# Optimization experiments

Hardware: AMD Instinct MI355X
Metric: run time of the kernel (lower is better)

Reference implementation:

```python
import jax, jax.numpy as jnp
import numpy as np
from jax import lax

S = 30      # num_sensors
FD = 200    # feature_dim
T = 1024    # signal length
B = 1024    # batch
NC = 7      # num_classes


def setup_inputs() -> dict:
    key = jax.random.key(0)
    ks = jax.random.split(key, 24)
    rn = lambda i, shape: jax.random.normal(ks[i], shape, jnp.float32) * 0.05
    # normalized adjacency with self-loops: D^-1/2 (A+I) D^-1/2
    rng = np.random.default_rng(0)
    A = (rng.random((S, S)) > 0.7).astype(np.float32)
    A = ((A + A.T) > 0).astype(np.float32)
    A_self = A + np.eye(S, dtype=np.float32)
    dinv = 1.0 / np.sqrt(A_self.sum(1))
    adj_self = jnp.asarray(dinv[:, None] * A_self * dinv[None, :])
    return dict(
        x=jax.random.normal(ks[0], (B, S, T), jnp.float32),
        adj_self=adj_self,
        Wc1=rn(1, (S, S, 3)), bc1=jnp.zeros((S,), jnp.float32),
        Wc2=rn(2, (S, S, 3)), bc2=jnp.zeros((S,), jnp.float32),
        Wt=rn(3, (T, FD)), bt=jnp.zeros((FD,), jnp.float32),
        Wa=rn(4, (FD, FD)),
        Wm1=rn(5, (FD, FD)), Wm2=rn(6, (FD, FD)), Wm3=rn(7, (FD, FD)),
        Wg1=rn(8, (FD, FD)), Wg2=rn(9, (FD, FD)),
        wg=rn(10, (FD, 3)),
        Wp1=rn(11, (FD, FD // 2)), Wp2=rn(12, (FD, FD // 2)), Wp3=rn(13, (FD, FD // 2)),
        Wl=rn(14, (FD, 150)), Wgl=rn(15, (FD, 150)),
        Ws1=rn(16, (S, S // 2)), Ws2=rn(17, (S // 2, S)),
        Wf1=rn(18, (300, 150)), Wf2=rn(19, (150, 300)),
        Wcls=rn(20, (S * 600, NC)), bcls=jnp.zeros((NC,), jnp.float32),
    )


def reference(x, adj_self, Wc1, bc1, Wc2, bc2, Wt, bt, Wa, Wm1, Wm2, Wm3,
              Wg1, Wg2, wg, Wp1, Wp2, Wp3, Wl, Wgl, Ws1, Ws2, Wf1, Wf2,
              Wcls, bcls):
    dn = ('NCH', 'OIH', 'NCH')
    # CNN feature extractor: [B,S,T] -> [B,S,FD]
    h = jax.nn.relu(lax.conv_general_dilated(x, Wc1, (1,), 'SAME', dimension_numbers=dn) + bc1[None, :, None])
    h = jax.nn.relu(lax.conv_general_dilated(h, Wc2, (1,), 'SAME', dimension_numbers=dn) + bc2[None, :, None])
    F2 = jax.nn.relu(jnp.einsum('bst,tf->bsf', h, Wt) + bt)
    # MGCN: learned feature adjacency + 3-order GCN (batched, replaces per-sample loop)
    A_F = jax.nn.softmax(jax.nn.relu(jnp.einsum('bif,fg,bjg->bij', F2, Wa, F2)), axis=-1)
    gc = lambda A, X, W: jax.nn.relu(jnp.einsum('bij,bjf,fg->big', A, X, W))
    x1 = gc(A_F, F2, Wm1)
    x2 = gc(A_F, x1, Wm2)
    x3 = gc(A_F, x2, Wm3)
    # signal GCN on physical adjacency (2-layer, eval mode so dropout is identity)
    h1 = jax.nn.relu(jnp.einsum('ij,bjf,fg->big', adj_self, F2, Wg1))
    x_sensor = jnp.einsum('ij,bjf,fg->big', adj_self, h1, Wg2)
    H1 = (x1 + x_sensor) * 0.5
    H2 = (x2 + x_sensor) * 0.5
    H3 = (x3 + x_sensor) * 0.5
    # adaptive aggregation: per-node softmax gate over 3 branches, project to FD//2 each -> 300
    scores = jnp.stack([jnp.einsum('bsf,f->bs', H, wg[:, k]) for k, H in enumerate((H1, H2, H3))], -1)
    g = jax.nn.softmax(scores, -1)  # [B,S,3]
    agg = lambda k, H, Wp: jnp.einsum('ij,bjf,fg->big', adj_self, g[..., k:k + 1] * H, Wp)
    G_h = jnp.concatenate([agg(0, H1, Wp1), agg(1, H2, Wp2), agg(2, H3, Wp3)], -1)  # [B,S,300]
    # LGFM: local (physical adj) + global (learned adj) -> 150+150
    loc = jax.nn.relu(jnp.einsum('ij,bjf,fg->big', adj_self, F2, Wl))
    glb = jax.nn.relu(jnp.einsum('bij,bjf,fg->big', A_F, F2, Wgl))
    G_v = jnp.concatenate([loc, glb], -1)  # [B,S,300]
    # cross squeeze-excitation: channel SE on G_h driven by G_v, feature SE on G_v driven by G_h
    wch = jax.nn.sigmoid(jax.nn.relu(G_v.mean(-1) @ Ws1) @ Ws2)   # [B,S]
    G_h_att = G_h * wch[:, :, None]
    wft = jax.nn.sigmoid(jax.nn.relu(G_h.mean(1) @ Wf1) @ Wf2)    # [B,300]
    G_v_att = G_v * wft[:, None, :]
    G = jnp.concatenate([G_h_att, G_v_att], -1).reshape(x.shape[0], -1)  # [B, S*600]
    return jax.nn.log_softmax(G @ Wcls + bcls, axis=-1)
```

## Files before the change

### kernel.cpp

```cpp
#include <hip/hip_runtime.h>
#include <math.h>

#define S   30
#define FD  200
#define TT  1024
#define BB  1024
#define NC  7

#define OFS_C1   0ull
#define OFS_F2   31457280ull
#define OFS_AF   0ull
#define OFS_GV   921600ull
#define OFS_GH   10137600ull
#define OFS_R    19691520ull
#define OFS_WT   28907520ull

__global__ __launch_bounds__(256) void k_conv1(
    const float* __restrict__ x,
    const float* __restrict__ Wc1, const float* __restrict__ bc1,
    float* __restrict__ C1) {
    const int c = blockIdx.x, b = blockIdx.y;
    const int t = threadIdx.x;
    const int t0 = c * 256;
    __shared__ float xb[S * 258];
// ... 77 lines not shown
__device__ inline void gemm_w4_pf(const float* Xl, int xstr, const float* __restrict__ W,
                                  int ct, int rt, float acc[][4]) {
    const float* wp = W + 4 * ct;
    float4 wreg[8];
#pragma unroll
    for (int u = 0; u < 8; u++) wreg[u] = *(const float4*)(wp + u * N);
#pragma unroll 1
    for (int kt = 0; kt < K / 8 - 1; kt++) {
        float4 wnxt[8];
#pragma unroll
        for (int u = 0; u < 8; u++) wnxt[u] = *(const float4*)(wp + (kt * 8 + 8 + u) * N);
#pragma unroll
        for (int m = 0; m < RPT; m++) {
            const float* xr = Xl + (rt * RPT + m) * xstr + kt * 8;
            float4 a0 = *(const float4*)(xr);
            float4 a1 = *(const float4*)(xr + 4);
            fma_tile8(a0, a1, wreg, acc[m]);
        }
#pragma unroll
        for (int u = 0; u < 8; u++) wreg[u] = wnxt[u];
    }
    {
        const int kb = K - 8;
#pragma unroll
        for (int m = 0; m < RPT; m++) {
            const float* xr = Xl + (rt * RPT + m) * xstr + kb;
            float4 a0 = *(const float4*)(xr);
            float4 a1 = *(const float4*)(xr + 4);
            fma_tile8(a0, a1, wreg, acc[m]);
        }
    }
}

template<int RPT, int N, int K>
__device__ inline void gemm_w4_pf_dual(const float* X0, const float* X1, int xstr,
                                       const float* __restrict__ W,
                                       int ct, int rt,
                                       float acc0[][4], float acc1[][4]) {
    const float* wp = W + 4 * ct;
    float4 wreg[8];
#pragma unroll
    for (int u = 0; u < 8; u++) wreg[u] = *(const float4*)(wp + u * N);
#pragma unroll 1
    for (int kt = 0; kt < K / 8 - 1; kt++) {
        float4 wnxt[8];
#pragma unroll
        for (int u = 0; u < 8; u++) wnxt[u] = *(const float4*)(wp + (kt * 8 + 8 + u) * N);
#pragma unroll
        for (int m = 0; m < RPT; m++) {
            const float* xr = X0 + (rt * RPT + m) * xstr + kt * 8;
            float4 a0 = *(const float4*)(xr);
            float4 a1 = *(const float4*)(xr + 4);
            fma_tile8(a0, a1, wreg, acc0[m]);
        }
#pragma unroll
        for (int m = 0; m < RPT; m++) {
            const float* xr = X1 + (rt * RPT + m) * xstr + kt * 8;
            float4 a0 = *(const float4*)(xr);
            float4 a1 = *(const float4*)(xr + 4);
            fma_tile8(a0, a1, wreg, acc1[m]);
        }
#pragma unroll
        for (int u = 0; u < 8; u++) wreg[u] = wnxt[u];
    }
    {
        const int kb = K - 8;
#pragma unroll
        for (int m = 0; m < RPT; m++) {
            const float* xr = X0 + (rt * RPT + m) * xstr + kb;
            float4 a0 = *(const float4*)(xr);
            float4 a1 = *(const float4*)(xr + 4);
            fma_tile8(a0, a1, wreg, acc0[m]);
        }
#pragma unroll
        for (int m = 0; m < RPT; m++) {
            const float* xr = X1 + (rt * RPT + m) * xstr + kb;
            float4 a0 = *(const float4*)(xr);
            float4 a1 = *(const float4*)(xr + 4);
            fma_tile8(a0, a1, wreg, acc1[m]);
        }
    }
}

template<int RPT>
__device__ inline void gemm_a32(const float* Al, const float* Xl, int xstr,
                                int ct, int rt, float acc[][4]) {
#pragma unroll
    for (int k4 = 0; k4 < 8; k4++) {
        float4 xv0 = *(const float4*)(Xl + (4 * k4 + 0) * xstr + 4 * ct);
        float4 xv1 = *(const float4*)(Xl + (4 * k4 + 1) * xstr + 4 * ct);
        float4 xv2 = *(const float4*)(Xl + (4 * k4 + 2) * xstr + 4 * ct);
        float4 xv3 = *(const float4*)(Xl + (4 * k4 + 3) * xstr + 4 * ct);
#pragma unroll
        for (int m = 0; m < RPT; m++) {
            float4 av = *(const float4*)(Al + (rt * RPT + m) * 32 + 4 * k4);
            FMA4(av.x, xv0, acc[m]);
            FMA4(av.y, xv1, acc[m]);
            FMA4(av.z, xv2, acc[m]);
            FMA4(av.w, xv3, acc[m]);
        }
    }
}

template<int RPT>
__device__ inline void gemm_a32_dual(const float* Al0, const float* X0,
                                     const float* Al1, const float* X1,
                                     int xstr, int ct, int rt,
                                     float acc0[][4], float acc1[][4]) {
#pragma unroll
    for (int k4 = 0; k4 < 8; k4++) {
        float4 x00 = *(const float4*)(X0 + (4 * k4 + 0) * xstr + 4 * ct);
        float4 x01 = *(const float4*)(X0 + (4 * k4 + 1) * xstr + 4 * ct);
        float4 x02 = *(const float4*)(X0 + (4 * k4 + 2) * xstr + 4 * ct);
        float4 x03 = *(const float4*)(X0 + (4 * k4 + 3) * xstr + 4 * ct);
        float4 x10 = *(const float4*)(X1 + (4 * k4 + 0) * xstr + 4 * ct);
        float4 x11 = *(const float4*)(X1 + (4 * k4 + 1) * xstr + 4 * ct);
        float4 x12 = *(const float4*)(X1 + (4 * k4 + 2) * xstr + 4 * ct);
        float4 x13 = *(const float4*)(X1 + (4 * k4 + 3) * xstr + 4 * ct);
#pragma unroll
        for (int m = 0; m < RPT; m++) {
            float4 av0 = *(const float4*)(Al0 + (rt * RPT + m) * 32 + 4 * k4);
            FMA4(av0.x, x00, acc0[m]);
            FMA4(av0.y, x01, acc0[m]);
            FMA4(av0.z, x02, acc0[m]);
            FMA4(av0.w, x03, acc0[m]);
            float4 av1 = *(const float4*)(Al1 + (rt * RPT + m) * 32 + 4 * k4);
            FMA4(av1.x, x10, acc1[m]);
            FMA4(av1.y, x11, acc1[m]);
            FMA4(av1.z, x12, acc1[m]);
            FMA4(av1.w, x13, acc1[m]);
        }
    }
}

__device__ inline void gemm_w150_pf(const float* Xl, const float* __restrict__ W,
                                    int ct2, int rt2, float acc[5][4], int off23) {
    const float* wp = W + 4 * ct2;
    float2 wa[8], wb[8];
#pragma unroll
    for (int u = 0; u < 8; u++) {
        wa[u] = *(const float2*)(wp + u * 150);
        wb[u] = *(const float2*)(wp + u * 150 + off23);
    }
#pragma unroll 1
    for (int kt = 0; kt < 24; kt++) {
        float2 na[8], nb[8];
#pragma unroll
        for (int u = 0; u < 8; u++) {
            int k = kt * 8 + 8 + u;
            na[u] = *(const float2*)(wp + k * 150);
            nb[u] = *(const float2*)(wp + k * 150 + off23);
        }
#pragma unroll
        for (int m = 0; m < 5; m++) {
            const float* xr = Xl + (rt2 * 5 + m) * FD + kt * 8;
            float4 a0 = *(const float4*)(xr);
            float4 a1 = *(const float4*)(xr + 4);
            float av[8] = {a0.x, a0.y, a0.z, a0.w, a1.x, a1.y, a1.z, a1.w};
#pragma unroll
            for (int u = 0; u < 8; u++) {
                acc[m][0] = fmaf(av[u], wa[u].x, acc[m][0]);
                acc[m][1] = fmaf(av[u], wa[u].y, acc[m][1]);
                acc[m][2] = fmaf(av[u], wb[u].x, acc[m][2]);
                acc[m][3] = fmaf(av[u], wb[u].y, acc[m][3]);
            }
        }
#pragma unroll
        for (int u = 0; u < 8; u++) { wa[u] = na[u]; wb[u] = nb[u]; }
    }
#pragma unroll
    for (int m = 0; m < 5; m++) {
        const float* xr = Xl + (rt2 * 5 + m) * FD + 192;
        float4 a0 = *(const float4*)(xr);
        float4 a1 = *(const float4*)(xr + 4);
        float av[8] = {a0.x, a0.y, a0.z, a0.w, a1.x, a1.y, a1.z, a1.w};
#pragma unroll
        for (int u = 0; u < 8; u++) {
            acc[m][0] = fmaf(av[u], wa[u].x, acc[m][0]);
            acc[m][1] = fmaf(av[u], wa[u].y, acc[m][1]);
            acc[m][2] = fmaf(av[u], wb[u].x, acc[m][2]);
            acc[m][3] = fmaf(av[u], wb[u].y, acc[m][3]);
        }
    }
}

__device__ inline void gemm_w150_pf_dual(const float* X0, const float* X1,
                                         const float* __restrict__ W,
                                         int ct2, int rt2,
                                         float acc0[5][4], float acc1[5][4], int off23) {
    const float* wp = W + 4 * ct2;
    float2 wa[8], wb[8];
#pragma unroll
    for (int u = 0; u < 8; u++) {
        wa[u] = *(const float2*)(wp + u * 150);
        wb[u] = *(const float2*)(wp + u * 150 + off23);
    }
#pragma unroll 1
    for (int kt = 0; kt < 24; kt++) {
        float2 na[8], nb[8];
#pragma unroll
        for (int u = 0; u < 8; u++) {
            int k = kt * 8 + 8 + u;
            na[u] = *(const float2*)(wp + k * 150);
            nb[u] = *(const float2*)(wp + k * 150 + off23);
        }
#pragma unroll
        for (int m = 0; m < 5; m++) {
            const float* xr = X0 + (rt2 * 5 + m) * FD + kt * 8;
            float4 a0 = *(const float4*)(xr);
            float4 a1 = *(const float4*)(xr + 4);
            float av[8] = {a0.x, a0.y, a0.z, a0.w, a1.x, a1.y, a1.z, a1.w};
#pragma unroll
            for (int u = 0; u < 8; u++) {
// ... 229 lines not shown
        float den = 0.f;
        for (int j = 0; j < S; j++) den += expf(scl0[t * 32 + j] - mx);
        float inv = 1.f / den;
        for (int j = 0; j < S; j++) scl0[t * 32 + j] = expf(scl0[t * 32 + j] - mx) * inv;
    } else if (t >= 64 && t < 64 + S) {
        int s = t - 64;
        float mx = -1e30f;
        for (int j = 0; j < S; j++) mx = fmaxf(mx, scl1[s * 32 + j]);
        float den = 0.f;
        for (int j = 0; j < S; j++) den += expf(scl1[s * 32 + j] - mx);
        float inv = 1.f / den;
        for (int j = 0; j < S; j++) scl1[s * 32 + j] = expf(scl1[s * 32 + j] - mx) * inv;
    }
    __syncthreads();
    for (int idx = t; idx < S * S; idx += 256) {
        int i = idx / S, j = idx % S;
        AF[(size_t)b0 * S * S + idx] = scl0[i * 32 + j];
        AF[(size_t)b1 * S * S + idx] = scl1[i * 32 + j];
    }
    zacc<6>(acc0); zacc<6>(acc1);
    if (t < 250) gemm_a32_dual<6>(adjl, A0, adjl, A1, FD, ct, rt, acc0, acc1);
    __syncthreads();
    if (t < 250) {
#pragma unroll
        for (int m = 0; m < 6; m++) {
            float4 o0 = {acc0[m][0], acc0[m][1], acc0[m][2], acc0[m][3]};
            float4 o1 = {acc1[m][0], acc1[m][1], acc1[m][2], acc1[m][3]};
            *(float4*)(Bu0 + (rt * 6 + m) * FD + 4 * ct) = o0;
            *(float4*)(Bu1 + (rt * 6 + m) * FD + 4 * ct) = o1;
        }
    }
    __syncthreads();
    const int ct2 = t % 38, rt2 = t / 38;
    const bool full = (4 * ct2 + 2) < 150;
    const int off23 = full ? 2 : -2;
    if (t < 228) {
        float a20[5][4], a21[5][4];
        zacc<5>(a20); zacc<5>(a21);
        gemm_w150_pf_dual(Bu0, Bu1, Wl, ct2, rt2, a20, a21, off23);
#pragma unroll
        for (int m = 0; m < 5; m++) {
            float* o0 = Gv + (size_t)(b0 * S + rt2 * 5 + m) * 300 + 4 * ct2;
            float* o1 = Gv + (size_t)(b1 * S + rt2 * 5 + m) * 300 + 4 * ct2;
            o0[0] = fmaxf(a20[m][0], 0.f); o0[1] = fmaxf(a20[m][1], 0.f);
            o1[0] = fmaxf(a21[m][0], 0.f); o1[1] = fmaxf(a21[m][1], 0.f);
            if (full) {
                o0[2] = fmaxf(a20[m][2], 0.f); o0[3] = fmaxf(a20[m][3], 0.f);
                o1[2] = fmaxf(a21[m][2], 0.f); o1[3] = fmaxf(a21[m][3], 0.f);
            }
        }
    }
    __syncthreads();
    zacc<6>(acc0); zacc<6>(acc1);
    if (t < 250) gemm_a32_dual<6>(scl0, A0, scl1, A1, FD, ct, rt, acc0, acc1);
    __syncthreads();
    if (t < 250) {
#pragma unroll
        for (int m = 0; m < 6; m++) {
            float4 o0 = {acc0[m][0], acc0[m][1], acc0[m][2], acc0[m][3]};
            float4 o1 = {acc1[m][0], acc1[m][1], acc1[m][2], acc1[m][3]};
            *(float4*)(Bu0 + (rt * 6 + m) * FD + 4 * ct) = o0;
            *(float4*)(Bu1 + (rt * 6 + m) * FD + 4 * ct) = o1;
        }
    }
    __syncthreads();
    if (t < 228) {
        float a20[5][4], a21[5][4];
        zacc<5>(a20); zacc<5>(a21);
        gemm_w150_pf_dual(Bu0, Bu1, Wgl, ct2, rt2, a20, a21, off23);
#pragma unroll
        for (int m = 0; m < 5; m++) {
            float* o0 = Gv + (size_t)(b0 * S + rt2 * 5 + m) * 300 + 150 + 4 * ct2;
            float* o1 = Gv + (size_t)(b1 * S + rt2 * 5 + m) * 300 + 150 + 4 * ct2;
            o0[0] = fmaxf(a20[m][0], 0.f); o0[1] = fmaxf(a20[m][1], 0.f);
            o1[0] = fmaxf(a21[m][0], 0.f); o1[1] = fmaxf(a21[m][1], 0.f);
            if (full) {
                o0[2] = fmaxf(a20[m][2], 0.f); o0[3] = fmaxf(a20[m][3], 0.f);
                o1[2] = fmaxf(a21[m][2], 0.f); o1[3] = fmaxf(a21[m][3], 0.f);
            }
        }
    }
}

__global__ __launch_bounds__(256, 2) void k_mgcn(
    const float* __restrict__ F2g, const float* __restrict__ AFg,
    const float* __restrict__ adj,
    const float* __restrict__ Wg1, const float* __restrict__ Wg2,
    const float* __restrict__ Wm1, const float* __restrict__ Wm2,
    const float* __restrict__ Wm3, const float* __restrict__ wg,
    const float* __restrict__ Wp1, const float* __restrict__ Wp2,
    const float* __restrict__ Wp3,
    float* __restrict__ Rws, float* __restrict__ Gh) {
    const int b0 = blockIdx.x * 2, b1 = b0 + 1;
    const int t = threadIdx.x;
    __shared__ float A0[32 * FD], A1[32 * FD];
    __shared__ float afl0[1024], afl1[1024];
    __shared__ float adjl[1024];
    __shared__ float sk[192];
    __shared__ float gl[192];
    const int ct = t % 50, rt = t / 50;
    const int ct3 = t % 25, rt3 = t / 25;

    for (int idx = t; idx < 1500; idx += 256) {
        *(float4*)(A0 + 4 * idx) = *(const float4*)(F2g + (size_t)b0 * S * FD + 4 * idx);
        *(float4*)(A1 + 4 * idx) = *(const float4*)(F2g + (size_t)b1 * S * FD + 4 * idx);
    }
    for (int idx = t; idx < 400; idx += 256) { A0[6000 + idx] = 0.f; A1[6000 + idx] = 0.f; }
    for (int idx = t; idx < 1024; idx += 256) {
        int r = idx >> 5, cc = idx & 31;
        bool in = (r < S && cc < S);
        afl0[idx] = in ? AFg[(size_t)b0 * S * S + r * S + cc] : 0.f;
        afl1[idx] = in ? AFg[(size_t)b1 * S * S + r * S + cc] : 0.f;
        adjl[idx] = in ? adj[r * S + cc] : 0.f;
    }
    if (t < 192) sk[t] = 0.f;
    __syncthreads();

    float acc0[6][4], acc1[6][4], xsr0[6][4], xsr1[6][4];

#define DZ() { zacc<6>(acc0); zacc<6>(acc1); }
#define DWRITE(RELU)                                                        \
    if (t < 250) {                                                          \
        _Pragma("unroll")                                                   \
        for (int m = 0; m < 6; m++) {                                       \
            float4 o0, o1;                                                  \
            o0.x = RELU ? fmaxf(acc0[m][0], 0.f) : acc0[m][0];              \
            o0.y = RELU ? fmaxf(acc0[m][1], 0.f) : acc0[m][1];              \
            o0.z = RELU ? fmaxf(acc0[m][2], 0.f) : acc0[m][2];              \
            o0.w = RELU ? fmaxf(acc0[m][3], 0.f) : acc0[m][3];              \
            o1.x = RELU ? fmaxf(acc1[m][0], 0.f) : acc1[m][0];              \
            o1.y = RELU ? fmaxf(acc1[m][1], 0.f) : acc1[m][1];              \
            o1.z = RELU ? fmaxf(acc1[m][2], 0.f) : acc1[m][2];              \
            o1.w = RELU ? fmaxf(acc1[m][3], 0.f) : acc1[m][3];              \
            *(float4*)(A0 + (rt * 6 + m) * FD + 4 * ct) = o0;               \
            *(float4*)(A1 + (rt * 6 + m) * FD + 4 * ct) = o1;               \
        }                                                                   \
    }

    DZ();
    if (t < 250) gemm_a32_dual<6>(adjl, A0, adjl, A1, FD, ct, rt, acc0, acc1);
    __syncthreads();
    DWRITE(false);
    __syncthreads();
    DZ();
    if (t < 250) gemm_w4_pf_dual<6, FD, FD>(A0, A1, FD, Wg1, ct, rt, acc0, acc1);
    __syncthreads();
    DWRITE(true);
    __syncthreads();
    DZ();
    if (t < 250) gemm_a32_dual<6>(adjl, A0, adjl, A1, FD, ct, rt, acc0, acc1);
    __syncthreads();
    DWRITE(false);
    __syncthreads();
    DZ();
    if (t < 250) gemm_w4_pf_dual<6, FD, FD>(A0, A1, FD, Wg2, ct, rt, acc0, acc1);
    __syncthreads();
#pragma unroll
    for (int m = 0; m < 6; m++) {
#pragma unroll
        for (int q = 0; q < 4; q++) { xsr0[m][q] = acc0[m][q]; xsr1[m][q] = acc1[m][q]; }
    }
    for (int idx = t; idx < 1500; idx += 256) {
        *(float4*)(A0 + 4 * idx) = *(const float4*)(F2g + (size_t)b0 * S * FD + 4 * idx);
        *(float4*)(A1 + 4 * idx) = *(const float4*)(F2g + (size_t)b1 * S * FD + 4 * idx);
    }
    __syncthreads();

    const float* Wm[3] = {Wm1, Wm2, Wm3};
    const float* Wp[3] = {Wp1, Wp2, Wp3};
#pragma unroll 1
    for (int k = 0; k < 3; k++) {
        DZ();
        if (t < 250) gemm_a32_dual<6>(afl0, A0, afl1, A1, FD, ct, rt, acc0, acc1);
        __syncthreads();
        DWRITE(false);
        __syncthreads();
        DZ();
        if (t < 250) gemm_w4_pf_dual<6, FD, FD>(A0, A1, FD, Wm[k], ct, rt, acc0, acc1);
        __syncthreads();
        if (t < 250) {
#pragma unroll
            for (int m = 0; m < 6; m++) {
#pragma unroll
                for (int q = 0; q < 4; q++) {
                    acc0[m][q] = fmaxf(acc0[m][q], 0.f);
                    acc1[m][q] = fmaxf(acc1[m][q], 0.f);
                }
            }
#pragma unroll
            for (int m = 0; m < 6; m++) {
                int row = rt * 6 + m;
                float wg0 = wg[(4 * ct + 0) * 3 + k], wg1v = wg[(4 * ct + 1) * 3 + k];
                float wg2v = wg[(4 * ct + 2) * 3 + k], wg3 = wg[(4 * ct + 3) * 3 + k];
                float h00 = 0.5f * (acc0[m][0] + xsr0[m][0]);
                float h01 = 0.5f * (acc0[m][1] + xsr0[m][1]);
                float h02 = 0.5f * (acc0[m][2] + xsr0[m][2]);
                float h03 = 0.5f * (acc0[m][3] + xsr0[m][3]);
                float4 o0 = {h00, h01, h02, h03};
                *(float4*)(A0 + row * FD + 4 * ct) = o0;
                atomicAdd(&sk[row * 3 + k],
                          h00 * wg0 + h01 * wg1v + h02 * wg2v + h03 * wg3);
                float h10 = 0.5f * (acc1[m][0] + xsr1[m][0]);
                float h11 = 0.5f * (acc1[m][1] + xsr1[m][1]);
                float h12 = 0.5f * (acc1[m][2] + xsr1[m][2]);
                float h13 = 0.5f * (acc1[m][3] + xsr1[m][3]);
                float4 o1 = {h10, h11, h12, h13};
                *(float4*)(A1 + row * FD + 4 * ct) = o1;
                atomicAdd(&sk[96 + row * 3 + k],
                          h10 * wg0 + h11 * wg1v + h12 * wg2v + h13 * wg3);
            }
        }
        __syncthreads();
        if (t < 250) {
            float a30[3][4], a31[3][4];
            zacc<3>(a30); zacc<3>(a31);
            gemm_w4_pf_dual<3, 100, FD>(A0, A1, FD, Wp[k], ct3, rt3, a30, a31);
#pragma unroll
            for (int m = 0; m < 3; m++) {
                float4 o0 = {a30[m][0], a30[m][1], a30[m][2], a30[m][3]};
                float4 o1 = {a31[m][0], a31[m][1], a31[m][2], a31[m][3]};
                *(float4*)(Rws + ((size_t)(k * BB + b0) * S + rt3 * 3 + m) * 100 + 4 * ct3) = o0;
                *(float4*)(Rws + ((size_t)(k * BB + b1) * S + rt3 * 3 + m) * 100 + 4 * ct3) = o1;
            }
        }
        __syncthreads();
        if (k < 2) {
            DWRITE(false);
            __syncthreads();
        }
    }

    if (t < S) {
        float a0 = sk[t * 3 + 0], a1 = sk[t * 3 + 1], a2 = sk[t * 3 + 2];
        float m = fmaxf(a0, fmaxf(a1, a2));
        float e0 = expf(a0 - m), e1 = expf(a1 - m), e2 = expf(a2 - m);
        float inv = 1.f / (e0 + e1 + e2);
        gl[t * 3 + 0] = e0 * inv; gl[t * 3 + 1] = e1 * inv; gl[t * 3 + 2] = e2 * inv;
    } else if (t >= 64 && t < 64 + S) {
        int s = t - 64;
        float a0 = sk[96 + s * 3 + 0], a1 = sk[96 + s * 3 + 1], a2 = sk[96 + s * 3 + 2];
        float m = fmaxf(a0, fmaxf(a1, a2));
        float e0 = expf(a0 - m), e1 = expf(a1 - m), e2 = expf(a2 - m);
        float inv = 1.f / (e0 + e1 + e2);
        gl[96 + s * 3 + 0] = e0 * inv; gl[96 + s * 3 + 1] = e1 * inv; gl[96 + s * 3 + 2] = e2 * inv;
    }
    __syncthreads();

#pragma unroll 1
    for (int k = 0; k < 3; k++) {
        for (int idx = t; idx < S * 100; idx += 256) {
            int row = idx / 100, col = idx % 100;
            A0[row * FD + col] = Rws[((size_t)(k * BB + b0) * S) * 100 + idx];
            A1[row * FD + col] = Rws[((size_t)(k * BB + b1) * S) * 100 + idx];
        }
        for (int idx = t; idx < 1024; idx += 256) {
            int cc = idx & 31;
            afl0[idx] = (cc < S) ? adjl[idx] * gl[cc * 3 + k] : 0.f;
            afl1[idx] = (cc < S) ? adjl[idx] * gl[96 + cc * 3 + k] : 0.f;
        }
        __syncthreads();
        if (t < 250) {
            float a30[3][4], a31[3][4];
            zacc<3>(a30); zacc<3>(a31);
            gemm_a32_dual<3>(afl0, A0, afl1, A1, FD, ct3, rt3, a30, a31);
#pragma unroll
            for (int m = 0; m < 3; m++) {
                float4 o0 = {a30[m][0], a30[m][1], a30[m][2], a30[m][3]};
                float4 o1 = {a31[m][0], a31[m][1], a31[m][2], a31[m][3]};
                *(float4*)(Gh + (size_t)(b0 * S + rt3 * 3 + m) * 300 + k * 100 + 4 * ct3) = o0;
                *(float4*)(Gh + (size_t)(b1 * S + rt3 * 3 + m) * 300 + k * 100 + 4 * ct3) = o1;
            }
        }
        __syncthreads();
    }
#undef DZ
#undef DWRITE
}

__global__ __launch_bounds__(256) void k_tw(const float* __restrict__ Wcls,
                                            float* __restrict__ WclsT) {
    int idx = blockIdx.x * 256 + threadIdx.x;
    if (idx < S * 600 * NC) {
        int i = idx / NC, c = idx % NC;
        WclsT[c * (S * 600) + i] = Wcls[idx];
    }
}

__global__ __launch_bounds__(256) void k_secls(
    const float* __restrict__ Gh, const float* __restrict__ Gv,
    const float* __restrict__ Ws1, const float* __restrict__ Ws2,
    const float* __restrict__ Wf1, const float* __restrict__ Wf2,
    const float* __restrict__ WclsT, const float* __restrict__ bcls,
    float* __restrict__ out) {
    const int b = blockIdx.x, t = threadIdx.x;
    __shared__ float red[NC][256];
    __shared__ float mrow[S];
    __shared__ float u[15];
    __shared__ float mb[300];
    __shared__ float v[150];
    __shared__ float wftl[300];
    __shared__ float wchl[S];
    if (t < S) {
        float a = 0.f;
        const float* gp = Gv + ((size_t)b * S + t) * 300;
        for (int j = 0; j < 300; j++) a += gp[j];
        mrow[t] = a * (1.f / 300.f);
    }
    for (int j = t; j < 300; j += 256) {
        float a = 0.f;
        for (int s = 0; s < S; s++) a += Gh[(size_t)b * S * 300 + s * 300 + j];
        mb[j] = a * (1.f / S);
    }
    __syncthreads();
    if (t < 15) {
        float a = 0.f;
        for (int i = 0; i < S; i++) a += mrow[i] * Ws1[i * 15 + t];
        u[t] = fmaxf(a, 0.f);
    }
    if (t >= 64 && t < 64 + 150) {
        int h = t - 64;
        float a = 0.f;
        for (int j = 0; j < 300; j++) a += mb[j] * Wf1[j * 150 + h];
        v[h] = fmaxf(a, 0.f);
    }
    __syncthreads();
    if (t < S) {
        float a = 0.f;
        for (int h = 0; h < 15; h++) a += u[h] * Ws2[h * 30 + t];
        wchl[t] = 1.f / (1.f + expf(-a));
    }
    for (int j = t; j < 300; j += 256) {
        float a = 0.f;
        for (int h = 0; h < 150; h++) a += v[h] * Wf2[h * 300 + j];
        wftl[j] = 1.f / (1.f + expf(-a));
    }
    __syncthreads();
    float acc[NC];
#pragma unroll
    for (int c = 0; c < NC; c++) acc[c] = 0.f;
    for (int i = t; i < S * 600; i += 256) {
        int s = i / 600, j = i % 600;
        float gval = (j < 300)
            ? Gh[(size_t)b * S * 300 + s * 300 + j] * wchl[s]
            : Gv[(size_t)b * S * 300 + s * 300 + (j - 300)] * wftl[j - 300];
#pragma unroll
        for (int c = 0; c < NC; c++)
            acc[c] = fmaf(gval, WclsT[c * (S * 600) + i], acc[c]);
    }
#pragma unroll
    for (int c = 0; c < NC; c++) red[c][t] = acc[c];
    __syncthreads();
    for (int off = 128; off > 0; off >>= 1) {
        if (t < off) {
#pragma unroll
            for (int c = 0; c < NC; c++) red[c][t] += red[c][t + off];
        }
        __syncthreads();
    }
    if (t == 0) {
        float lg[NC];
        float mx = -1e30f;
#pragma unroll
        for (int c = 0; c < NC; c++) { lg[c] = red[c][0] + bcls[c]; mx = fmaxf(mx, lg[c]); }
        float den = 0.f;
#pragma unroll
        for (int c = 0; c < NC; c++) den += expf(lg[c] - mx);
        float lden = logf(den) + mx;
#pragma unroll
        for (int c = 0; c < NC; c++) out[b * NC + c] = lg[c] - lden;
    }
}

extern "C" void kernel_launch(void* const* d_in, const int* in_sizes, int n_in,
                              void* d_out, int out_size, void* d_ws, size_t ws_size,
                              hipStream_t stream) {
    const float* x    = (const float*)d_in[0];
    const float* adj  = (const float*)d_in[1];
    const float* Wc1  = (const float*)d_in[2];
    const float* bc1  = (const float*)d_in[3];
    const float* Wc2  = (const float*)d_in[4];
    const float* bc2  = (const float*)d_in[5];
    const float* Wt   = (const float*)d_in[6];
    const float* bt   = (const float*)d_in[7];
    const float* Wa   = (const float*)d_in[8];
    const float* Wm1  = (const float*)d_in[9];
    const float* Wm2  = (const float*)d_in[10];
    const float* Wm3  = (const float*)d_in[11];
    const float* Wg1  = (const float*)d_in[12];
    const float* Wg2  = (const float*)d_in[13];
    const float* wg   = (const float*)d_in[14];
    const float* Wp1  = (const float*)d_in[15];
    const float* Wp2  = (const float*)d_in[16];
    const float* Wp3  = (const float*)d_in[17];
    const float* Wl   = (const float*)d_in[18];
    const float* Wgl  = (const float*)d_in[19];
    const float* Ws1  = (const float*)d_in[20];
    const float* Ws2  = (const float*)d_in[21];
    const float* Wf1  = (const float*)d_in[22];
    const float* Wf2  = (const float*)d_in[23];
    const float* Wcls = (const float*)d_in[24];
    const float* bcls = (const float*)d_in[25];

    float* ws    = (float*)d_ws;
    float* C1    = ws + OFS_C1;
    float* F2    = ws + OFS_F2;
    float* AF    = ws + OFS_AF;
    float* GV    = ws + OFS_GV;
    float* GH    = ws + OFS_GH;
    float* RWS   = ws + OFS_R;
    float* WCLST = ws + OFS_WT;
    float* out   = (float*)d_out;

    k_conv1<<<dim3(4, BB), 256, 0, stream>>>(x, Wc1, bc1, C1);
    k_f2d<<<BB / 2, 256, 0, stream>>>(C1, Wc2, bc2, Wt, bt, F2);
    k_tw<<<(S * 600 * NC + 255) / 256, 256, 0, stream>>>(Wcls, WCLST);
    k_att2<<<BB / 2, 256, 0, stream>>>(F2, Wa, adj, Wl, Wgl, AF, GV);
    k_mgcn<<<BB / 2, 256, 0, stream>>>(F2, AF, adj, Wg1, Wg2, Wm1, Wm2, Wm3, wg,
                                       Wp1, Wp2, Wp3, RWS, GH);
    k_secls<<<BB, 256, 0, stream>>>(GH, GV, Ws1, Ws2, Wf1, Wf2, WCLST, bcls, out);
}
```

Before: 1.135 ms.

## Process four batch samples per block in MGCN kernel to reuse weight loads

The MGCN kernel now handles four samples per block instead of two, with quad variants of the adjacency and weight GEMM helpers so each prefetched weight tile feeds four samples. This halves weight traffic per sample and halves the block count. In exchange, shared memory rises to about 120 KB and register pressure roughly doubles (four accumulator sets plus four saved residuals), so launch bounds drop to one block per SM. Only 256 blocks are launched, which risks spills and poor occupancy.

```diff
diff --git a/kernel.cpp b/kernel.cpp
--- a/kernel.cpp
+++ b/kernel.cpp
@@ -183,6 +183,70 @@
     }
 }
 
+template<int RPT, int N, int K>
+__device__ inline void gemm_w4_pf_quad(const float* X0, const float* X1,
+                                       const float* X2, const float* X3, int xstr,
+                                       const float* __restrict__ W,
+                                       int ct, int rt,
+                                       float acc0[][4], float acc1[][4],
+                                       float acc2[][4], float acc3[][4]) {
+    const float* wp = W + 4 * ct;
+    float4 wreg[8];
+#pragma unroll
+    for (int u = 0; u < 8; u++) wreg[u] = *(const float4*)(wp + u * N);
+#pragma unroll 1
+    for (int kt = 0; kt < K / 8 - 1; kt++) {
+        float4 wnxt[8];
+#pragma unroll
+        for (int u = 0; u < 8; u++) wnxt[u] = *(const float4*)(wp + (kt * 8 + 8 + u) * N);
+#pragma unroll
+        for (int m = 0; m < RPT; m++) {
+            const float* xr = X0 + (rt * RPT + m) * xstr + kt * 8;
+            fma_tile8(*(const float4*)(xr), *(const float4*)(xr + 4), wreg, acc0[m]);
+        }
+#pragma unroll
+        for (int m = 0; m < RPT; m++) {
+            const float* xr = X1 + (rt * RPT + m) * xstr + kt * 8;
+            fma_tile8(*(const float4*)(xr), *(const float4*)(xr + 4), wreg, acc1[m]);
+        }
+#pragma unroll
+        for (int m = 0; m < RPT; m++) {
+            const float* xr = X2 + (rt * RPT + m) * xstr + kt * 8;
+            fma_tile8(*(const float4*)(xr), *(const float4*)(xr + 4), wreg, acc2[m]);
+        }
+#pragma unroll
+        for (int m = 0; m < RPT; m++) {
+            const float* xr = X3 + (rt * RPT + m) * xstr + kt * 8;
+            fma_tile8(*(const float4*)(xr), *(const float4*)(xr + 4), wreg, acc3[m]);
+        }
+#pragma unroll
+        for (int u = 0; u < 8; u++) wreg[u] = wnxt[u];
+    }
+    {
+        const int kb = K - 8;
+#pragma unroll
+        for (int m = 0; m < RPT; m++) {
+            const float* xr = X0 + (rt * RPT + m) * xstr + kb;
+            fma_tile8(*(const float4*)(xr), *(const float4*)(xr + 4), wreg, acc0[m]);
+        }
+#pragma unroll
+        for (int m = 0; m < RPT; m++) {
+            const float* xr = X1 + (rt * RPT + m) * xstr + kb;
+            fma_tile8(*(const float4*)(xr), *(const float4*)(xr + 4), wreg, acc1[m]);
+        }
+#pragma unroll
+        for (int m = 0; m < RPT; m++) {
+            const float* xr = X2 + (rt * RPT + m) * xstr + kb;
+            fma_tile8(*(const float4*)(xr), *(const float4*)(xr + 4), wreg, acc2[m]);
+        }
+#pragma unroll
+        for (int m = 0; m < RPT; m++) {
+            const float* xr = X3 + (rt * RPT + m) * xstr + kb;
+            fma_tile8(*(const float4*)(xr), *(const float4*)(xr + 4), wreg, acc3[m]);
+        }
+    }
+}
+
 template<int RPT>
 __device__ inline void gemm_a32(const float* Al, const float* Xl, int xstr,
                                 int ct, int rt, float acc[][4]) {
@@ -230,6 +294,75 @@
             FMA4(av1.y, x11, acc1[m]);
             FMA4(av1.z, x12, acc1[m]);
             FMA4(av1.w, x13, acc1[m]);
+        }
+    }
+}
+
+template<int RPT>
+__device__ inline void gemm_a32_quad(const float* Al0, const float* X0,
+                                     const float* Al1, const float* X1,
+                                     const float* Al2, const float* X2,
+                                     const float* Al3, const float* X3,
+                                     int xstr, int ct, int rt,
+                                     float acc0[][4], float acc1[][4],
+                                     float acc2[][4], float acc3[][4]) {
+#pragma unroll
+    for (int k4 = 0; k4 < 8; k4++) {
+        {
+            float4 x0 = *(const float4*)(X0 + (4 * k4 + 0) * xstr + 4 * ct);
+            float4 x1 = *(const float4*)(X0 + (4 * k4 + 1) * xstr + 4 * ct);
+            float4 x2 = *(const float4*)(X0 + (4 * k4 + 2) * xstr + 4 * ct);
+            float4 x3 = *(const float4*)(X0 + (4 * k4 + 3) * xstr + 4 * ct);
+#pragma unroll
+            for (int m = 0; m < RPT; m++) {
+                float4 av = *(const float4*)(Al0 + (rt * RPT + m) * 32 + 4 * k4);
+                FMA4(av.x, x0, acc0[m]);
+                FMA4(av.y, x1, acc0[m]);
+                FMA4(av.z, x2, acc0[m]);
+                FMA4(av.w, x3, acc0[m]);
+            }
+        }
+        {
+            float4 x0 = *(const float4*)(X1 + (4 * k4 + 0) * xstr + 4 * ct);
+            float4 x1 = *(const float4*)(X1 + (4 * k4 + 1) * xstr + 4 * ct);
+            float4 x2 = *(const float4*)(X1 + (4 * k4 + 2) * xstr + 4 * ct);
+            float4 x3 = *(const float4*)(X1 + (4 * k4 + 3) * xstr + 4 * ct);
+#pragma unroll
+            for (int m = 0; m < RPT; m++) {
+                float4 av = *(const float4*)(Al1 + (rt * RPT + m) * 32 + 4 * k4);
+                FMA4(av.x, x0, acc1[m]);
+                FMA4(av.y, x1, acc1[m]);
+                FMA4(av.z, x2, acc1[m]);
+                FMA4(av.w, x3, acc1[m]);
+            }
+        }
+        {
+            float4 x0 = *(const float4*)(X2 + (4 * k4 + 0) * xstr + 4 * ct);
+            float4 x1 = *(const float4*)(X2 + (4 * k4 + 1) * xstr + 4 * ct);
+            float4 x2 = *(const float4*)(X2 + (4 * k4 + 2) * xstr + 4 * ct);
+            float4 x3 = *(const float4*)(X2 + (4 * k4 + 3) * xstr + 4 * ct);
+#pragma unroll
+            for (int m = 0; m < RPT; m++) {
+                float4 av = *(const float4*)(Al2 + (rt * RPT + m) * 32 + 4 * k4);
+                FMA4(av.x, x0, acc2[m]);
+                FMA4(av.y, x1, acc2[m]);
+                FMA4(av.z, x2, acc2[m]);
+                FMA4(av.w, x3, acc2[m]);
+            }
+        }
+        {
+            float4 x0 = *(const float4*)(X3 + (4 * k4 + 0) * xstr + 4 * ct);
+            float4 x1 = *(const float4*)(X3 + (4 * k4 + 1) * xstr + 4 * ct);
+            float4 x2 = *(const float4*)(X3 + (4 * k4 + 2) * xstr + 4 * ct);
+            float4 x3 = *(const float4*)(X3 + (4 * k4 + 3) * xstr + 4 * ct);
+#pragma unroll
+            for (int m = 0; m < RPT; m++) {
+                float4 av = *(const float4*)(Al3 + (rt * RPT + m) * 32 + 4 * k4);
+                FMA4(av.x, x0, acc3[m]);
+                FMA4(av.y, x1, acc3[m]);
+                FMA4(av.z, x2, acc3[m]);
+                FMA4(av.w, x3, acc3[m]);
+            }
         }
     }
 }
@@ -625,7 +758,7 @@
     }
 }
 
-__global__ __launch_bounds__(256, 2) void k_mgcn(
+__global__ __launch_bounds__(256, 1) void k_mgcn4(
     const float* __restrict__ F2g, const float* __restrict__ AFg,
     const float* __restrict__ adj,
     const float* __restrict__ Wg1, const float* __restrict__ Wg2,
@@ -634,39 +767,47 @@
     const float* __restrict__ Wp1, const float* __restrict__ Wp2,
     const float* __restrict__ Wp3,
     float* __restrict__ Rws, float* __restrict__ Gh) {
-    const int b0 = blockIdx.x * 2, b1 = b0 + 1;
+    const int b0 = blockIdx.x * 4;
     const int t = threadIdx.x;
-    __shared__ float A0[32 * FD], A1[32 * FD];
-    __shared__ float afl0[1024], afl1[1024];
+    __shared__ float A0[32 * FD], A1[32 * FD], A2[32 * FD], A3[32 * FD];
+    __shared__ float afl0[1024], afl1[1024], afl2[1024], afl3[1024];
     __shared__ float adjl[1024];
-    __shared__ float sk[192];
-    __shared__ float gl[192];
+    __shared__ float sk[384];
+    __shared__ float gl[384];
     const int ct = t % 50, rt = t / 50;
     const int ct3 = t % 25, rt3 = t / 25;
 
     for (int idx = t; idx < 1500; idx += 256) {
-        *(float4*)(A0 + 4 * idx) = *(const float4*)(F2g + (size_t)b0 * S * FD + 4 * idx);
-        *(float4*)(A1 + 4 * idx) = *(const float4*)(F2g + (size_t)b1 * S * FD + 4 * idx);
-    }
-    for (int idx = t; idx < 400; idx += 256) { A0[6000 + idx] = 0.f; A1[6000 + idx] = 0.f; }
+        *(float4*)(A0 + 4 * idx) = *(const float4*)(F2g + (size_t)(b0 + 0) * S * FD + 4 * idx);
+        *(float4*)(A1 + 4 * idx) = *(const float4*)(F2g + (size_t)(b0 + 1) * S * FD + 4 * idx);
+        *(float4*)(A2 + 4 * idx) = *(const float4*)(F2g + (size_t)(b0 + 2) * S * FD + 4 * idx);
+        *(float4*)(A3 + 4 * idx) = *(const float4*)(F2g + (size_t)(b0 + 3) * S * FD + 4 * idx);
+    }
+    for (int idx = t; idx < 400; idx += 256) {
+        A0[6000 + idx] = 0.f; A1[6000 + idx] = 0.f;
+        A2[6000 + idx] = 0.f; A3[6000 + idx] = 0.f;
+    }
     for (int idx = t; idx < 1024; idx += 256) {
         int r = idx >> 5, cc = idx & 31;
         bool in = (r < S && cc < S);
-        afl0[idx] = in ? AFg[(size_t)b0 * S * S + r * S + cc] : 0.f;
-        afl1[idx] = in ? AFg[(size_t)b1 * S * S + r * S + cc] : 0.f;
+        afl0[idx] = in ? AFg[(size_t)(b0 + 0) * S * S + r * S + cc] : 0.f;
+        afl1[idx] = in ? AFg[(size_t)(b0 + 1) * S * S + r * S + cc] : 0.f;
+        afl2[idx] = in ? AFg[(size_t)(b0 + 2) * S * S + r * S + cc] : 0.f;
+        afl3[idx] = in ? AFg[(size_t)(b0 + 3) * S * S + r * S + cc] : 0.f;
         adjl[idx] = in ? adj[r * S + cc] : 0.f;
     }
-    if (t < 192) sk[t] = 0.f;
-    __syncthreads();
-
-    float acc0[6][4], acc1[6][4], xsr0[6][4], xsr1[6][4];
-
-#define DZ() { zacc<6>(acc0); zacc<6>(acc1); }
-#define DWRITE(RELU)                                                        \
+    for (int idx = t; idx < 384; idx += 256) sk[idx] = 0.f;
+    __syncthreads();
+
+    float acc0[6][4], acc1[6][4], acc2[6][4], acc3[6][4];
+    float xsr0[6][4], xsr1[6][4], xsr2[6][4], xsr3[6][4];
+
+#define QZ() { zacc<6>(acc0); zacc<6>(acc1); zacc<6>(acc2); zacc<6>(acc3); }
+#define QWRITE(RELU)                                                        \
     if (t < 250) {                                                          \
         _Pragma("unroll")                                                   \
         for (int m = 0; m < 6; m++) {                                       \
-            float4 o0, o1;                                                  \
+            float4 o0, o1, o2, o3;                                          \
             o0.x = RELU ? fmaxf(acc0[m][0], 0.f) : acc0[m][0];              \
             o0.y = RELU ? fmaxf(acc0[m][1], 0.f) : acc0[m][1];              \
             o0.z = RELU ? fmaxf(acc0[m][2], 0.f) : acc0[m][2];              \
@@ -675,37 +816,56 @@
             o1.y = RELU ? fmaxf(acc1[m][1], 0.f) : acc1[m][1];              \
             o1.z = RELU ? fmaxf(acc1[m][2], 0.f) : acc1[m][2];              \
             o1.w = RELU ? fmaxf(acc1[m][3], 0.f) : acc1[m][3];              \
+            o2.x = RELU ? fmaxf(acc2[m][0], 0.f) : acc2[m][0];              \
+            o2.y = RELU ? fmaxf(acc2[m][1], 0.f) : acc2[m][1];              \
+            o2.z = RELU ? fmaxf(acc2[m][2], 0.f) : acc2[m][2];              \
+            o2.w = RELU ? fmaxf(acc2[m][3], 0.f) : acc2[m][3];              \
+            o3.x = RELU ? fmaxf(acc3[m][0], 0.f) : acc3[m][0];              \
+            o3.y = RELU ? fmaxf(acc3[m][1], 0.f) : acc3[m][1];              \
+            o3.z = RELU ? fmaxf(acc3[m][2], 0.f) : acc3[m][2];              \
+            o3.w = RELU ? fmaxf(acc3[m][3], 0.f) : acc3[m][3];              \
             *(float4*)(A0 + (rt * 6 + m) * FD + 4 * ct) = o0;               \
             *(float4*)(A1 + (rt * 6 + m) * FD + 4 * ct) = o1;               \
+            *(float4*)(A2 + (rt * 6 + m) * FD + 4 * ct) = o2;               \
+            *(float4*)(A3 + (rt * 6 + m) * FD + 4 * ct) = o3;               \
         }                                                                   \
     }
 
-    DZ();
-    if (t < 250) gemm_a32_dual<6>(adjl, A0, adjl, A1, FD, ct, rt, acc0, acc1);
-    __syncthreads();
-    DWRITE(false);
-    __syncthreads();
-    DZ();
-    if (t < 250) gemm_w4_pf_dual<6, FD, FD>(A0, A1, FD, Wg1, ct, rt, acc0, acc1);
-    __syncthreads();
-    DWRITE(true);
-    __syncthreads();
-    DZ();
-    if (t < 250) gemm_a32_dual<6>(adjl, A0, adjl, A1, FD, ct, rt, acc0, acc1);
-    __syncthreads();
-    DWRITE(false);
-    __syncthreads();
-    DZ();
-    if (t < 250) gemm_w4_pf_dual<6, FD, FD>(A0, A1, FD, Wg2, ct, rt, acc0, acc1);
+    QZ();
+    if (t < 250) gemm_a32_quad<6>(adjl, A0, adjl, A1, adjl, A2, adjl, A3,
+                                  FD, ct, rt, acc0, acc1, acc2, acc3);
+    __syncthreads();
+    QWRITE(false);
+    __syncthreads();
+    QZ();
+    if (t < 250) gemm_w4_pf_quad<6, FD, FD>(A0, A1, A2, A3, FD, Wg1, ct, rt,
+                                            acc0, acc1, acc2, acc3);
+    __syncthreads();
+    QWRITE(true);
+    __syncthreads();
+    QZ();
+    if (t < 250) gemm_a32_quad<6>(adjl, A0, adjl, A1, adjl, A2, adjl, A3,
+                                  FD, ct, rt, acc0, acc1, acc2, acc3);
+    __syncthreads();
+    QWRITE(false);
+    __syncthreads();
+    QZ();
+    if (t < 250) gemm_w4_pf_quad<6, FD, FD>(A0, A1, A2, A3, FD, Wg2, ct, rt,
+                                            acc0, acc1, acc2, acc3);
     __syncthreads();
 #pragma unroll
     for (int m = 0; m < 6; m++) {
 #pragma unroll
-        for (int q = 0; q < 4; q++) { xsr0[m][q] = acc0[m][q]; xsr1[m][q] = acc1[m][q]; }
+        for (int q = 0; q < 4; q++) {
+            xsr0[m][q] = acc0[m][q]; xsr1[m][q] = acc1[m][q];
+            xsr2[m][q] = acc2[m][q]; xsr3[m][q] = acc3[m][q];
+        }
     }
     for (int idx = t; idx < 1500; idx += 256) {
-        *(float4*)(A0 + 4 * idx) = *(const float4*)(F2g + (size_t)b0 * S * FD + 4 * idx);
-        *(float4*)(A1 + 4 * idx) = *(const float4*)(F2g + (size_t)b1 * S * FD + 4 * idx);
+        *(float4*)(A0 + 4 * idx) = *(const float4*)(F2g + (size_t)(b0 + 0) * S * FD + 4 * idx);
+        *(float4*)(A1 + 4 * idx) = *(const float4*)(F2g + (size_t)(b0 + 1) * S * FD + 4 * idx);
+        *(float4*)(A2 + 4 * idx) = *(const float4*)(F2g + (size_t)(b0 + 2) * S * FD + 4 * idx);
+        *(float4*)(A3 + 4 * idx) = *(const float4*)(F2g + (size_t)(b0 + 3) * S * FD + 4 * idx);
     }
     __syncthreads();
 
@@ -713,13 +873,15 @@
     const float* Wp[3] = {Wp1, Wp2, Wp3};
 #pragma unroll 1
     for (int k = 0; k < 3; k++) {
-        DZ();
-        if (t < 250) gemm_a32_dual<6>(afl0, A0, afl1, A1, FD, ct, rt, acc0, acc1);
+        QZ();
+        if (t < 250) gemm_a32_quad<6>(afl0, A0, afl1, A1, afl2, A2, afl3, A3,
+                                      FD, ct, rt, acc0, acc1, acc2, acc3);
         __syncthreads();
-        DWRITE(false);
+        QWRITE(false);
         __syncthreads();
-        DZ();
-        if (t < 250) gemm_w4_pf_dual<6, FD, FD>(A0, A1, FD, Wm[k], ct, rt, acc0, acc1);
+        QZ();
+        if (t < 250) gemm_w4_pf_quad<6, FD, FD>(A0, A1, A2, A3, FD, Wm[k], ct, rt,
+                                                acc0, acc1, acc2, acc3);
         __syncthreads();
         if (t < 250) {
 #pragma unroll
@@ -728,6 +890,8 @@
                 for (int q = 0; q < 4; q++) {
                     acc0[m][q] = fmaxf(acc0[m][q], 0.f);
                     acc1[m][q] = fmaxf(acc1[m][q], 0.f);
+                    acc2[m][q] = fmaxf(acc2[m][q], 0.f);
+                    acc3[m][q] = fmaxf(acc3[m][q], 0.f);
                 }
             }
 #pragma unroll
@@ -735,89 +899,112 @@
                 int row = rt * 6 + m;
                 float wg0 = wg[(4 * ct + 0) * 3 + k], wg1v = wg[(4 * ct + 1) * 3 + k];
                 float wg2v = wg[(4 * ct + 2) * 3 + k], wg3 = wg[(4 * ct + 3) * 3 + k];
-                float h00 = 0.5f * (acc0[m][0] + xsr0[m][0]);
-                float h01 = 0.5f * (acc0[m][1] + xsr0[m][1]);
-                float h02 = 0.5f * (acc0[m][2] + xsr0[m][2]);
-                float h03 = 0.5f * (acc0[m][3] + xsr0[m][3]);
-                float4 o0 = {h00, h01, h02, h03};
-                *(float4*)(A0 + row * FD + 4 * ct) = o0;
-                atomicAdd(&sk[row * 3 + k],
-                          h00 * wg0 + h01 * wg1v + h02 * wg2v + h03 * wg3);
-                float h10 = 0.5f * (acc1[m][0] + xsr1[m][0]);
-                float h11 = 0.5f * (acc1[m][1] + xsr1[m][1]);
-                float h12 = 0.5f * (acc1[m][2] + xsr1[m][2]);
-                float h13 = 0.5f * (acc1[m][3] + xsr1[m][3]);
-                float4 o1 = {h10, h11, h12, h13};
-                *(float4*)(A1 + row * FD + 4 * ct) = o1;
-                atomicAdd(&sk[96 + row * 3 + k],
-                          h10 * wg0 + h11 * wg1v + h12 * wg2v + h13 * wg3);
+                float h0, h1, h2, h3;
+                h0 = 0.5f * (acc0[m][0] + xsr0[m][0]);
+                h1 = 0.5f * (acc0[m][1] + xsr0[m][1]);
+                h2 = 0.5f * (acc0[m][2] + xsr0[m][2]);
+                h3 = 0.5f * (acc0[m][3] + xsr0[m][3]);
+                { float4 o = {h0, h1, h2, h3}; *(float4*)(A0 + row * FD + 4 * ct) = o; }
+                atomicAdd(&sk[row * 3 + k], h0 * wg0 + h1 * wg1v + h2 * wg2v + h3 * wg3);
+                h0 = 0.5f * (acc1[m][0] + xsr1[m][0]);
+                h1 = 0.5f * (acc1[m][1] + xsr1[m][1]);
+                h2 = 0.5f * (acc1[m][2] + xsr1[m][2]);
+                h3 = 0.5f * (acc1[m][3] + xsr1[m][3]);
+                { float4 o = {h0, h1, h2, h3}; *(float4*)(A1 + row * FD + 4 * ct) = o; }
+                atomicAdd(&sk[96 + row * 3 + k], h0 * wg0 + h1 * wg1v + h2 * wg2v + h3 * wg3);
+                h0 = 0.5f * (acc2[m][0] + xsr2[m][0]);
+                h1 = 0.5f * (acc2[m][1] + xsr2[m][1]);
+                h2 = 0.5f * (acc2[m][2] + xsr2[m][2]);
+                h3 = 0.5f * (acc2[m][3] + xsr2[m][3]);
+                { float4 o = {h0, h1, h2, h3}; *(float4*)(A2 + row * FD + 4 * ct) = o; }
+                atomicAdd(&sk[192 + row * 3 + k], h0 * wg0 + h1 * wg1v + h2 * wg2v + h3 * wg3);
+                h0 = 0.5f * (acc3[m][0] + xsr3[m][0]);
+                h1 = 0.5f * (acc3[m][1] + xsr3[m][1]);
+                h2 = 0.5f * (acc3[m][2] + xsr3[m][2]);
+                h3 = 0.5f * (acc3[m][3] + xsr3[m][3]);
+                { float4 o = {h0, h1, h2, h3}; *(float4*)(A3 + row * FD + 4 * ct) = o; }
+                atomicAdd(&sk[288 + row * 3 + k], h0 * wg0 + h1 * wg1v + h2 * wg2v + h3 * wg3);
             }
         }
         __syncthreads();
         if (t < 250) {
-            float a30[3][4], a31[3][4];
-            zacc<3>(a30); zacc<3>(a31);
-            gemm_w4_pf_dual<3, 100, FD>(A0, A1, FD, Wp[k], ct3, rt3, a30, a31);
+            float a30[3][4], a31[3][4], a32[3][4], a33[3][4];
+            zacc<3>(a30); zacc<3>(a31); zacc<3>(a32); zacc<3>(a33);
+            gemm_w4_pf_quad<3, 100, FD>(A0, A1, A2, A3, FD, Wp[k], ct3, rt3,
+                                        a30, a31, a32, a33);
 #pragma unroll
             for (int m = 0; m < 3; m++) {
                 float4 o0 = {a30[m][0], a30[m][1], a30[m][2], a30[m][3]};
                 float4 o1 = {a31[m][0], a31[m][1], a31[m][2], a31[m][3]};
-                *(float4*)(Rws + ((size_t)(k * BB + b0) * S + rt3 * 3 + m) * 100 + 4 * ct3) = o0;
-                *(float4*)(Rws + ((size_t)(k * BB + b1) * S + rt3 * 3 + m) * 100 + 4 * ct3) = o1;
+                float4 o2 = {a32[m][0], a32[m][1], a32[m][2], a32[m][3]};
+                float4 o3 = {a33[m][0], a33[m][1], a33[m][2], a33[m][3]};
+                *(float4*)(Rws + ((size_t)(k * BB + b0 + 0) * S + rt3 * 3 + m) * 100 + 4 * ct3) = o0;
+                *(float4*)(Rws + ((size_t)(k * BB + b0 + 1) * S + rt3 * 3 + m) * 100 + 4 * ct3) = o1;
+                *(float4*)(Rws + ((size_t)(k * BB + b0 + 2) * S + rt3 * 3 + m) * 100 + 4 * ct3) = o2;
+                *(float4*)(Rws + ((size_t)(k * BB + b0 + 3) * S + rt3 * 3 + m) * 100 + 4 * ct3) = o3;
             }
         }
         __syncthreads();
         if (k < 2) {
-            DWRITE(false);
+            QWRITE(false);
             __syncthreads();
         }
     }
 
-    if (t < S) {
-        float a0 = sk[t * 3 + 0], a1 = sk[t * 3 + 1], a2 = sk[t * 3 + 2];
-        float m = fmaxf(a0, fmaxf(a1, a2));
-        float e0 = expf(a0 - m), e1 = expf(a1 - m), e2 = expf(a2 - m);
-        float inv = 1.f / (e0 + e1 + e2);
-        gl[t * 3 + 0] = e0 * inv; gl[t * 3 + 1] = e1 * inv; gl[t * 3 + 2] = e2 * inv;
-    } else if (t >= 64 && t < 64 + S) {
-        int s = t - 64;
-        float a0 = sk[96 + s * 3 + 0], a1 = sk[96 + s * 3 + 1], a2 = sk[96 + s * 3 + 2];
-        float m = fmaxf(a0, fmaxf(a1, a2));
-        float e0 = expf(a0 - m), e1 = expf(a1 - m), e2 = expf(a2 - m);
-        float inv = 1.f / (e0 + e1 + e2);
-        gl[96 + s * 3 + 0] = e0 * inv; gl[96 + s * 3 + 1] = e1 * inv; gl[96 + s * 3 + 2] = e2 * inv;
+    {
+        int grp = t >> 6, lane = t & 63;
+        if (lane < S) {
+            int base = grp * 96;
+            float a0 = sk[base + lane * 3 + 0];
+            float a1 = sk[base + lane * 3 + 1];
+            float a2 = sk[base + lane * 3 + 2];
+            float m = fmaxf(a0, fmaxf(a1, a2));
+            float e0 = expf(a0 - m), e1 = expf(a1 - m), e2 = expf(a2 - m);
+            float inv = 1.f / (e0 + e1 + e2);
+            gl[base + lane * 3 + 0] = e0 * inv;
+            gl[base + lane * 3 + 1] = e1 * inv;
+            gl[base + lane * 3 + 2] = e2 * inv;
+        }
     }
     __syncthreads();
 
 #pragma unroll 1
     for (int k = 0; k < 3; k++) {
-        for (int idx = t; idx < S * 100; idx += 256) {
-            int row = idx / 100, col = idx % 100;
-            A0[row * FD + col] = Rws[((size_t)(k * BB + b0) * S) * 100 + idx];
-            A1[row * FD + col] = Rws[((size_t)(k * BB + b1) * S) * 100 + idx];
+        for (int idx = t; idx < 4 * S * 100; idx += 256) {
+            int h = idx / 3000, r = idx % 3000;
+            int row = r / 100, col = r % 100;
+            float* Ah = (h == 0) ? A0 : (h == 1) ? A1 : (h == 2) ? A2 : A3;
+            Ah[row * FD + col] = Rws[((size_t)(k * BB + b0 + h) * S) * 100 + r];
         }
         for (int idx = t; idx < 1024; idx += 256) {
             int cc = idx & 31;
             afl0[idx] = (cc < S) ? adjl[idx] * gl[cc * 3 + k] : 0.f;
             afl1[idx] = (cc < S) ? adjl[idx] * gl[96 + cc * 3 + k] : 0.f;
+            afl2[idx] = (cc < S) ? adjl[idx] * gl[192 + cc * 3 + k] : 0.f;
+            afl3[idx] = (cc < S) ? adjl[idx] * gl[288 + cc * 3 + k] : 0.f;
         }
         __syncthreads();
         if (t < 250) {
-            float a30[3][4], a31[3][4];
-            zacc<3>(a30); zacc<3>(a31);
-            gemm_a32_dual<3>(afl0, A0, afl1, A1, FD, ct3, rt3, a30, a31);
+            float a30[3][4], a31[3][4], a32[3][4], a33[3][4];
+            zacc<3>(a30); zacc<3>(a31); zacc<3>(a32); zacc<3>(a33);
+            gemm_a32_quad<3>(afl0, A0, afl1, A1, afl2, A2, afl3, A3,
+                             FD, ct3, rt3, a30, a31, a32, a33);
 #pragma unroll
             for (int m = 0; m < 3; m++) {
                 float4 o0 = {a30[m][0], a30[m][1], a30[m][2], a30[m][3]};
                 float4 o1 = {a31[m][0], a31[m][1], a31[m][2], a31[m][3]};
-                *(float4*)(Gh + (size_t)(b0 * S + rt3 * 3 + m) * 300 + k * 100 + 4 * ct3) = o0;
-                *(float4*)(Gh + (size_t)(b1 * S + rt3 * 3 + m) * 300 + k * 100 + 4 * ct3) = o1;
+                float4 o2 = {a32[m][0], a32[m][1], a32[m][2], a32[m][3]};
+                float4 o3 = {a33[m][0], a33[m][1], a33[m][2], a33[m][3]};
+                *(float4*)(Gh + (size_t)((b0 + 0) * S + rt3 * 3 + m) * 300 + k * 100 + 4 * ct3) = o0;
+                *(float4*)(Gh + (size_t)((b0 + 1) * S + rt3 * 3 + m) * 300 + k * 100 + 4 * ct3) = o1;
+                *(float4*)(Gh + (size_t)((b0 + 2) * S + rt3 * 3 + m) * 300 + k * 100 + 4 * ct3) = o2;
+                *(float4*)(Gh + (size_t)((b0 + 3) * S + rt3 * 3 + m) * 300 + k * 100 + 4 * ct3) = o3;
             }
         }
         __syncthreads();
     }
-#undef DZ
-#undef DWRITE
+#undef QZ
+#undef QWRITE
 }
 
 __global__ __launch_bounds__(256) void k_tw(const float* __restrict__ Wcls,
@@ -958,7 +1145,7 @@
     k_f2d<<<BB / 2, 256, 0, stream>>>(C1, Wc2, bc2, Wt, bt, F2);
     k_tw<<<(S * 600 * NC + 255) / 256, 256, 0, stream>>>(Wcls, WCLST);
     k_att2<<<BB / 2, 256, 0, stream>>>(F2, Wa, adj, Wl, Wgl, AF, GV);
-    k_mgcn<<<BB / 2, 256, 0, stream>>>(F2, AF, adj, Wg1, Wg2, Wm1, Wm2, Wm3, wg,
-                                       Wp1, Wp2, Wp3, RWS, GH);
+    k_mgcn4<<<BB / 4, 256, 0, stream>>>(F2, AF, adj, Wg1, Wg2, Wm1, Wm2, Wm3, wg,
+                                        Wp1, Wp2, Wp3, RWS, GH);
     k_secls<<<BB, 256, 0, stream>>>(GH, GV, Ws1, Ws2, Wf1, Wf2, WCLST, bcls, out);
 }
```

Result: slower. 1.261 ms (+11.0%).
